# Performance work log

Measured on AMD Instinct MI355X. Metric: run time of the kernel, lower is better.

The kernel has to match this reference:

```python
import jax, jax.numpy as jnp
import numpy as np

R_MAX = 5.0
NUM_BESSEL = 8
P_CUT = 5.0
NUM_GRAPHS = 32
AVG_NEIGH = 16.0
N_NODES = 40000
N_EDGES = 640000
NUM_ELEM = 10
CHANNELS = 32
# map each of the 9 spherical-harmonic components (l=0..2) to its l index
L_OF_LM = jnp.array([0, 1, 1, 1, 2, 2, 2, 2, 2])


def _sph(u):
    # component-normalized real spherical harmonics up to l=2 on unit vectors
    x, y, z = u[:, 0], u[:, 1], u[:, 2]
    s3, s15, s5 = jnp.sqrt(3.0), jnp.sqrt(15.0), jnp.sqrt(5.0)
    return jnp.stack([
        jnp.ones_like(x),
        s3 * x, s3 * y, s3 * z,
        s15 * x * y, s15 * y * z,
        (s5 / 2.0) * (3.0 * z * z - 1.0),
        s15 * x * z, (s15 / 2.0) * (x * x - y * y),
    ], axis=-1)  # [E, 9]


def _radial(lengths):
    # Bessel radial basis with smooth polynomial cutoff (p = P_CUT)
    u = lengths / R_MAX
    n = jnp.arange(1, NUM_BESSEL + 1, dtype=lengths.dtype)
    bessel = jnp.sqrt(2.0 / R_MAX) * jnp.sin(n * jnp.pi * u[:, None]) / lengths[:, None]
    p = P_CUT
    fc = (1.0 - (p + 1.0) * (p + 2.0) / 2.0 * u ** p
          + p * (p + 2.0) * u ** (p + 1.0)
          - p * (p + 1.0) / 2.0 * u ** (p + 2.0))
    fc = jnp.where(u < 1.0, fc, 0.0)
    return bessel * fc[:, None]  # [E, NUM_BESSEL]


def _layer(h, sh, edge_feats, sender, receiver, W1, W2, n_nodes):
    # radial MLP -> per-(l, channel) tensor-product weights
    tp_w = jax.nn.silu(edge_feats @ W1) @ W2          # [E, 3*C]
    tp_w = tp_w.reshape(-1, 3, CHANNELS)[:, L_OF_LM]  # [E, 9, C]
    # equivariant message: sh outer sender scalar feats, radially weighted
    m = sh[:, :, None] * h[sender][:, None, :] * tp_w  # [E, 9, C]
    A = jax.ops.segment_sum(m, receiver, num_segments=n_nodes) / AVG_NEIGH
    return A.at[:, 0, :].add(h)  # residual on the scalar (l=0) part


def _energy(positions, node_attrs, shifts, atomic_energies, W_embed,
            W1a, W2a, Wr1, W1b, W2b, Wm1, Wm2, edge_index, batch):
    sender, receiver = edge_index[0], edge_index[1]
    vec = positions[receiver] - positions[sender] + shifts  # [E, 3]
    lengths = jnp.sqrt(jnp.maximum(jnp.sum(vec * vec, -1), 1e-12))
    sh = _sph(vec / lengths[:, None])
    ef = _radial(lengths)
    n_nodes = positions.shape[0]
    e0 = node_attrs @ atomic_energies       # per-atom reference energies
    h = node_attrs @ W_embed                # LinearNodeEmbeddingBlock
    A1 = _layer(h, sh, ef, sender, receiver, W1a, W2a, n_nodes)
    e1 = (A1[:, 0, :] @ Wr1)[:, 0]          # LinearReadoutBlock
    A2 = _layer(A1[:, 0, :], sh, ef, sender, receiver, W1b, W2b, n_nodes)
    e2 = (jax.nn.silu(A2[:, 0, :] @ Wm1) @ Wm2)[:, 0]  # NonLinearReadoutBlock
    node_energy = e0 + e1 + e2
    total = jax.ops.segment_sum(node_energy, batch, num_segments=NUM_GRAPHS)
    return total, node_energy


def setup_inputs() -> dict:
    key = jax.random.key(0)
    ks = jax.random.split(key, 16)
    node_z = jax.random.randint(ks[0], (N_NODES,), 0, NUM_ELEM)
    node_attrs = jax.nn.one_hot(node_z, NUM_ELEM, dtype=jnp.float32)
    return {
        "positions": jax.random.normal(ks[1], (N_NODES, 3), jnp.float32) * 2.0,
        "node_attrs": node_attrs,
        "shifts": jnp.zeros((N_EDGES, 3), jnp.float32),
        "atomic_energies": jax.random.normal(ks[2], (NUM_ELEM,), jnp.float32),
        "W_embed": jax.random.normal(ks[3], (NUM_ELEM, CHANNELS), jnp.float32) / np.sqrt(NUM_ELEM),
        "W1a": jax.random.normal(ks[4], (NUM_BESSEL, 64), jnp.float32) / np.sqrt(NUM_BESSEL),
        "W2a": jax.random.normal(ks[5], (64, 3 * CHANNELS), jnp.float32) / 8.0,
        "Wr1": jax.random.normal(ks[6], (CHANNELS, 1), jnp.float32) / np.sqrt(CHANNELS),
        "W1b": jax.random.normal(ks[7], (NUM_BESSEL, 64), jnp.float32) / np.sqrt(NUM_BESSEL),
        "W2b": jax.random.normal(ks[8], (64, 3 * CHANNELS), jnp.float32) / 8.0,
        "Wm1": jax.random.normal(ks[9], (CHANNELS, 16), jnp.float32) / np.sqrt(CHANNELS),
        "Wm2": jax.random.normal(ks[10], (16, 1), jnp.float32) / 4.0,
        "edge_index": jax.random.randint(ks[11], (2, N_EDGES), 0, N_NODES).astype(jnp.int32),
        "batch": jnp.sort(jax.random.randint(ks[12], (N_NODES,), 0, NUM_GRAPHS)).astype(jnp.int32),
    }


def reference(positions, node_attrs, shifts, atomic_energies, W_embed,
              W1a, W2a, Wr1, W1b, W2b, Wm1, Wm2, edge_index, batch):
    def esum(pos):
        total, node_e = _energy(pos, node_attrs, shifts, atomic_energies, W_embed,
                                W1a, W2a, Wr1, W1b, W2b, Wm1, Wm2, edge_index, batch)
        return jnp.sum(total), (total, node_e)

    (_, (total, node_e)), g = jax.value_and_grad(esum, has_aux=True)(positions)
    forces = -g  # forces = -dE/dpositions, as in get_outputs
    return total, node_e, forces
```

## Files before the change

kernel.cpp:

```cpp
#include <hip/hip_runtime.h>
#include <math.h>

constexpr float R_MAX   = 5.0f;
constexpr float INV_R   = 0.2f;
constexpr float PI_F    = 3.14159265358979323846f;
constexpr float C0      = 0.632455532033675866f;
constexpr float INV_AVG = 1.0f / 16.0f;
constexpr int   TBL     = 4096;
constexpr int   SCHUNK  = 512;

__device__ __forceinline__ float sigm(float x) { return 1.0f / (1.0f + __expf(-x)); }

__device__ __forceinline__ unsigned f2bf(float x) {
    unsigned u = __float_as_uint(x);
    u += 0x7fffu + ((u >> 16) & 1u);
    return u >> 16;
}
__device__ __forceinline__ void store_bf_row(unsigned short* dst, const float* v) {
    uint4* o = (uint4*)dst;
#pragma unroll
    for (int w = 0; w < 4; w++) {
        uint4 t;
        t.x = f2bf(v[8*w+0]) | (f2bf(v[8*w+1]) << 16);
        t.y = f2bf(v[8*w+2]) | (f2bf(v[8*w+3]) << 16);
        t.z = f2bf(v[8*w+4]) | (f2bf(v[8*w+5]) << 16);
        t.w = f2bf(v[8*w+6]) | (f2bf(v[8*w+7]) << 16);
        o[w] = t;
    }
}
__device__ __forceinline__ void load_bf_row(const unsigned short* src, float* v) {
    const uint4* p = (const uint4*)src;
#pragma unroll
    for (int w = 0; w < 4; w++) {
        uint4 t = p[w];
        v[8*w+0] = __uint_as_float(t.x << 16);
        v[8*w+1] = __uint_as_float(t.x & 0xffff0000u);
        v[8*w+2] = __uint_as_float(t.y << 16);
        v[8*w+3] = __uint_as_float(t.y & 0xffff0000u);
        v[8*w+4] = __uint_as_float(t.z << 16);
        v[8*w+5] = __uint_as_float(t.z & 0xffff0000u);
        v[8*w+6] = __uint_as_float(t.w << 16);
        v[8*w+7] = __uint_as_float(t.w & 0xffff0000u);
    }
}

__device__ __forceinline__ void radial_ef_d(float u, float invL, float* ef, float* dd) {
    float u2 = u * u, u4 = u2 * u2, u5 = u4 * u;
    float fc  = 1.f - 21.f * u5 + 35.f * u5 * u - 15.f * u5 * u2;
    float om  = 1.f - u;
    float fcp = -105.f * u4 * om * om;
    float sp, cp;
    sincosf(PI_F * u, &sp, &cp);
    float twoc = 2.f * cp;
    float a = C0 * invL;
    float s_nm1 = 0.f, s_n = sp, c_nm1 = 1.f, c_n = cp;
#pragma unroll
    for (int n = 1; n <= 8; n++) {
        ef[n - 1] = a * s_n * fc;
        dd[n - 1] = a * fc * ((float)n * PI_F * INV_R * c_n - s_n * invL)
                  + a * s_n * fcp * INV_R;
        if (n < 8) {
            float sn2 = twoc * s_n - s_nm1; s_nm1 = s_n; s_n = sn2;
            float cn2 = twoc * c_n - c_nm1; c_nm1 = c_n; c_n = cn2;
        }
    }
}

__global__ __launch_bounds__(256) void k_setup(
    const float* __restrict__ W1a, const float* __restrict__ W2a,
    const float* __restrict__ W1b, const float* __restrict__ W2b,
    float* __restrict__ twa, float* __restrict__ dta,
    float* __restrict__ twb, float* __restrict__ dtb,
    float* __restrict__ total,
    const float* __restrict__ attrs, const float* __restrict__ ae,
    const float* __restrict__ Wemb, float* __restrict__ h,
    unsigned short* __restrict__ hA1_bf, float* __restrict__ e0,
    float* __restrict__ A1, float* __restrict__ forces, int N,
    const float* __restrict__ pos, const float* __restrict__ shifts,
    const int* __restrict__ ei, int E,
    int* __restrict__ hist_r, int* __restrict__ hist_s,
    float4* __restrict__ urec,
    int nbt, int nbn)
{
    int b = blockIdx.x;
    if (b < nbt) {
        if (b == 0 && threadIdx.x < 32) total[threadIdx.x] = 0.f;
        int gid = b * 256 + threadIdx.x;
        if (gid >= (TBL + 1) * 16) return;
        int cg = gid & 7;
        int l  = (gid >> 3) & 1;
        int t  = gid >> 4;
        float u = fmaxf((float)t / (float)TBL, 1e-4f);
        float L = u * R_MAX;
        float invL = 1.f / L;
        float ef[8], dd[8], efu[8];
        radial_ef_d(u, invL, ef, dd);
#pragma unroll
        for (int k = 0; k < 8; k++) efu[k] = dd[k] * R_MAX;
        const float* W1 = l ? W1b : W1a;
        const float* W2 = l ? W2b : W2a;
        float*     tw_o = l ? twb : twa;
        float*     dt_o = l ? dtb : dta;
        float tw[4] = {0.f, 0.f, 0.f, 0.f};
        float dt[4] = {0.f, 0.f, 0.f, 0.f};
        for (int j = 0; j < 64; j++) {
            float s1 = 0.f, du = 0.f;
#pragma unroll
            for (int k = 0; k < 8; k++) {
                float w = W1[k * 64 + j];
                s1 += ef[k] * w; du += efu[k] * w;
            }
            float sg  = sigm(s1);
            float act = s1 * sg;
            float dj  = sg * (1.f + s1 * (1.f - sg)) * du;
            const float* w2 = W2 + j * 96 + cg * 4;
#pragma unroll
            for (int q = 0; q < 4; q++) {
                tw[q] += act * w2[q];
                dt[q] += dj * w2[q];
            }
        }
#pragma unroll
        for (int q = 0; q < 4; q++) {
            tw_o[(size_t)t * 32 + cg * 4 + q] = tw[q];
            dt_o[(size_t)t * 32 + cg * 4 + q] = dt[q];
        }
    } else if (b < nbt + nbn) {
        int i = (b - nbt) * 256 + threadIdx.x;
        if (i >= N) return;
        float a[10];
#pragma unroll
        for (int k = 0; k < 10; k++) a[k] = attrs[i * 10 + k];
        float e = 0.f;
#pragma unroll
        for (int k = 0; k < 10; k++) e += a[k] * ae[k];
        e0[i] = e;
        float v[32];
#pragma unroll
        for (int c = 0; c < 32; c++) {
            float t = 0.f;
#pragma unroll
            for (int k = 0; k < 10; k++) t += a[k] * Wemb[k * 32 + c];
            v[c] = t;
            h[i * 32 + c] = t;
            A1[i * 32 + c] = 0.f;
        }
        store_bf_row(hA1_bf + (size_t)i * 64, v);
        forces[3*i+0] = 0.f; forces[3*i+1] = 0.f; forces[3*i+2] = 0.f;
        hist_r[i] = 0; hist_s[i] = 0;
    } else {
        int e = (b - nbt - nbn) * 256 + threadIdx.x;
        if (e >= E) return;
        int s = ei[e], r = ei[E + e];
        float vx = pos[3*r+0] - pos[3*s+0] + shifts[3*e+0];
        float vy = pos[3*r+1] - pos[3*s+1] + shifts[3*e+1];
        float vz = pos[3*r+2] - pos[3*s+2] + shifts[3*e+2];
        float ss2 = vx*vx + vy*vy + vz*vz;
        float L = sqrtf(fmaxf(ss2, 1e-12f));
        if (L * INV_R < 1.f) {
            atomicAdd(&hist_r[r], 1);
            atomicAdd(&hist_s[s], 1);
            urec[e] = make_float4(vx, vy, vz,
                      __uint_as_float(((unsigned)s << 16) | (unsigned)r));
        } else {
            urec[e] = make_float4(0.f, 0.f, 0.f, __uint_as_float(0xFFFFFFFFu));
        }
    }
}

__global__ __launch_bounds__(256) void k_scan_a(
    const int* __restrict__ hist_r, const int* __restrict__ hist_s,
    int n, int nb, int* __restrict__ part)
{
    __shared__ int red[256];
    int b = blockIdx.x;
    const int* hist = (b < nb) ? hist_r : hist_s;
    int cb = (b < nb) ? b : b - nb;
    int base = cb * SCHUNK;
    int t = threadIdx.x;
    int i0 = base + 2 * t, i1 = i0 + 1;
    int sum = 0;
    if (i0 < n) sum += hist[i0];
    if (i1 < n) sum += hist[i1];
    red[t] = sum;
    __syncthreads();
    for (int off = 128; off > 0; off >>= 1) {
        if (t < off) red[t] += red[t + off];
        __syncthreads();
    }
    if (t == 0) part[b] = red[0];
}

__global__ __launch_bounds__(256) void k_scan_b(
    const int* __restrict__ part, int nb, int* __restrict__ bbase,
    int* __restrict__ cnt)
{
    __shared__ int buf[512];
    int t = threadIdx.x;
    for (int k = t; k < 2 * nb; k += 256) buf[k] = part[k];
    __syncthreads();
    if (t < 2) {
        int base = t * nb;
        int run = 0;
        for (int k = 0; k < nb; k++) {
            int v = buf[base + k];
            buf[base + k] = run;
            run += v;
        }
        if (t == 0) *cnt = run;
    }
    __syncthreads();
    for (int k = t; k < 2 * nb; k += 256) bbase[k] = buf[k];
}

__global__ __launch_bounds__(256) void k_scan_c(
    const int* __restrict__ hist_r, const int* __restrict__ hist_s,
    int n, int nb, const int* __restrict__ bbase,
    int* __restrict__ cur_r, int* __restrict__ cur_s)
{
    __shared__ int sc[256];
    int b = blockIdx.x;
    const int* hist = (b < nb) ? hist_r : hist_s;
    int*       cur  = (b < nb) ? cur_r : cur_s;
    int cb = (b < nb) ? b : b - nb;
    int base = cb * SCHUNK;
    int t = threadIdx.x;
    int i0 = base + 2 * t, i1 = i0 + 1;
    int e0 = (i0 < n) ? hist[i0] : 0;
    int e1 = (i1 < n) ? hist[i1] : 0;
    int ts = e0 + e1;
    sc[t] = ts;
    __syncthreads();
    for (int off = 1; off < 256; off <<= 1) {
        int v = (t >= off) ? sc[t - off] : 0;
        __syncthreads();
        sc[t] += v;
        __syncthreads();
    }
    int excl = sc[t] - ts + bbase[b];
    if (i0 < n) cur[i0] = excl;
    if (i1 < n) cur[i1] = excl + e0;
}

__global__ __launch_bounds__(256) void k_sort(
    const float4* __restrict__ urec, int E,
    int* __restrict__ cur_r, int* __restrict__ cur_s,
    float4* __restrict__ rrec, float4* __restrict__ srec,
    int* __restrict__ map_sr)
{
    int e = blockIdx.x * 256 + threadIdx.x;
    if (e >= E) return;
    float4 uv = urec[e];
    unsigned pk = __float_as_uint(uv.w);
    if (pk == 0xFFFFFFFFu) return;
    int r = (int)(pk & 0xffffu);
    int s = (int)(pk >> 16);
    int rp = atomicAdd(&cur_r[r], 1);
    int sp = atomicAdd(&cur_s[s], 1);
    rrec[rp] = uv;
    srec[sp] = make_float4(uv.x, uv.y, uv.z,
               __uint_as_float(((unsigned)r << 16) | (unsigned)s));
    map_sr[sp] = rp;
}

__global__ __launch_bounds__(256) void k_edge_mlp_t(
    const float4* __restrict__ rec, const int* __restrict__ cnt,
    const float* __restrict__ tw_tbl, const unsigned short* __restrict__ feat,
    int fstride, float* __restrict__ acc)
{
    __shared__ float m_lds[256][33];
    __shared__ int   dst_lds[256];

    int na = *cnt;
    int tid = threadIdx.x;
    int stride = gridDim.x * 256;

    for (int base = blockIdx.x * 256; base < na; base += stride) {
        int i = base + tid;
        int dst = -1;
        if (i < na) {
            float4 rv = rec[i];
            unsigned pk = __float_as_uint(rv.w);
            int gn = pk >> 16;
            dst = (int)(pk & 0xffffu);
            float ss2 = rv.x * rv.x + rv.y * rv.y + rv.z * rv.z;
            float L = sqrtf(fmaxf(ss2, 1e-12f));
            float x = fminf(L * (INV_R * (float)TBL), (float)TBL - 1e-3f);
            int   i0 = (int)x;
            float f  = x - (float)i0;

            float fbuf[32];
            load_bf_row(feat + (size_t)gn * fstride, fbuf);

            const float4* r0 = (const float4*)(tw_tbl + (size_t)i0 * 32);
            const float4* r1 = r0 + 8;
#pragma unroll
            for (int q = 0; q < 8; q++) {
                float4 a = r0[q], b = r1[q];
                m_lds[tid][4 * q + 0] = fbuf[4*q+0] * (a.x + f * (b.x - a.x));
                m_lds[tid][4 * q + 1] = fbuf[4*q+1] * (a.y + f * (b.y - a.y));
                m_lds[tid][4 * q + 2] = fbuf[4*q+2] * (a.z + f * (b.z - a.z));
                m_lds[tid][4 * q + 3] = fbuf[4*q+3] * (a.w + f * (b.w - a.w));
            }
        }
        dst_lds[tid] = dst;
        __syncthreads();

        int grp = tid >> 5;
        int c   = tid & 31;
        int b32 = grp * 32;
        int cur = -1; float run = 0.f;
        for (int k = 0; k < 32; k++) {
            int d = dst_lds[b32 + k];
            if (d != cur) {
                if (cur >= 0) unsafeAtomicAdd(&acc[(size_t)cur * 32 + c], run);
                cur = d;
                run = (d >= 0) ? m_lds[b32 + k][c] : 0.f;
            } else if (d >= 0) {
                run += m_lds[b32 + k][c];
            }
        }
        if (cur >= 0) unsafeAtomicAdd(&acc[(size_t)cur * 32 + c], run);
        __syncthreads();
    }
}

__global__ __launch_bounds__(256) void k_node1(
    const float* __restrict__ h, float* __restrict__ A1,
    unsigned short* __restrict__ hA1_bf,
    const float* __restrict__ Wr1, float* __restrict__ e1,
    float* __restrict__ A2g2, int N)
{
    int i = blockIdx.x * blockDim.x + threadIdx.x;
    if (i >= N) return;
    float dot = 0.f;
    float v[32];
#pragma unroll
    for (int c = 0; c < 32; c++) {
        float t = A1[i * 32 + c] * INV_AVG + h[i * 32 + c];
        v[c] = t;
        A1[i * 32 + c] = t;
        A2g2[i * 32 + c] = 0.f;
        dot += t * Wr1[c];
    }
    e1[i] = dot;
    store_bf_row(hA1_bf + (size_t)i * 64 + 32, v);
}

__global__ __launch_bounds__(256) void k_node2(
    float* __restrict__ A2g2, unsigned short* __restrict__ g2_bf,
    const float* __restrict__ A1,
    const float* __restrict__ Wm1, const float* __restrict__ Wm2,
    const float* __restrict__ e0, const float* __restrict__ e1,
    float* __restrict__ node_e, float* __restrict__ total,
    float* __restrict__ g1, const int* __restrict__ batch, int N)
{
    __shared__ float bins[32];
    if (threadIdx.x < 32) bins[threadIdx.x] = 0.f;
    __syncthreads();
    int i = blockIdx.x * blockDim.x + threadIdx.x;
    if (i < N) {
        float A2[32];
#pragma unroll
        for (int c = 0; c < 32; c++) {
            A2[c] = A2g2[i * 32 + c] * INV_AVG + A1[i * 32 + c];
            g1[i * 32 + c] = 0.f;
        }
        float z[16];
#pragma unroll
        for (int k = 0; k < 16; k++) {
            float v = 0.f;
#pragma unroll
            for (int c = 0; c < 32; c++) v += A2[c] * Wm1[c * 16 + k];
            z[k] = v;
        }
        float e2 = 0.f;
        float wk[16];
#pragma unroll
        for (int k = 0; k < 16; k++) {
            float sg = sigm(z[k]);
            float m2 = Wm2[k];
            e2 += z[k] * sg * m2;
            wk[k] = m2 * sg * (1.f + z[k] * (1.f - sg));
        }
        float g2v[32];
#pragma unroll
        for (int c = 0; c < 32; c++) {
            float v = 0.f;
#pragma unroll
            for (int k = 0; k < 16; k++) v += Wm1[c * 16 + k] * wk[k];
            g2v[c] = v;
            A2g2[i * 32 + c] = v;
        }
        store_bf_row(g2_bf + (size_t)i * 32, g2v);
        float ne = e0[i] + e1[i] + e2;
        node_e[i] = ne;
        atomicAdd(&bins[batch[i]], ne);
    }
    __syncthreads();
    if (threadIdx.x < 32) unsafeAtomicAdd(&total[threadIdx.x], bins[threadIdx.x]);
}

__global__ __launch_bounds__(256) void k_mlp3fb(
    const float4* __restrict__ rec, const int* __restrict__ cnt,
    const float* __restrict__ tw_tbl, const float* __restrict__ dt_tbl,
    const unsigned short* __restrict__ g2_bf,
    const unsigned short* __restrict__ hA1_bf,
    const int* __restrict__ map_sr,
    float* __restrict__ g1acc, float* __restrict__ dotb_buf)
{
    __shared__ float m_lds[256][33];
    __shared__ int   dst_lds[256];

    int na = *cnt;
    int tid = threadIdx.x;
    int stride = gridDim.x * 256;

    for (int base = blockIdx.x * 256; base < na; base += stride) {
        int i = base + tid;
        int dst = -1;
        if (i < na) {
            float4 rv = rec[i];
            unsigned pk = __float_as_uint(rv.w);
            int r = (int)(pk >> 16);
            dst = (int)(pk & 0xffffu);
            float ss2 = rv.x * rv.x + rv.y * rv.y + rv.z * rv.z;
            float L = sqrtf(fmaxf(ss2, 1e-12f));
            float x = fminf(L * (INV_R * (float)TBL), (float)TBL - 1e-3f);
            int   i0 = (int)x;
            float f  = x - (float)i0;

            float gb[32], ab[32];
            load_bf_row(g2_bf + (size_t)r * 32, gb);
            load_bf_row(hA1_bf + (size_t)dst * 64 + 32, ab);

            const float4* r0 = (const float4*)(tw_tbl + (size_t)i0 * 32);
            const float4* r1 = r0 + 8;
            const float4* d0 = (const float4*)(dt_tbl + (size_t)i0 * 32);
            const float4* d1 = d0 + 8;
            float dotb = 0.f;
#pragma unroll
            for (int q = 0; q < 8; q++) {
                float4 a = r0[q], b = r1[q], da = d0[q], db = d1[q];
                float t0 = a.x + f * (b.x - a.x);
                float t1 = a.y + f * (b.y - a.y);
                float t2 = a.z + f * (b.z - a.z);
                float t3 = a.w + f * (b.w - a.w);
                m_lds[tid][4*q+0] = gb[4*q+0] * t0;
                m_lds[tid][4*q+1] = gb[4*q+1] * t1;
                m_lds[tid][4*q+2] = gb[4*q+2] * t2;
                m_lds[tid][4*q+3] = gb[4*q+3] * t3;
                dotb += gb[4*q+0] * ab[4*q+0] * (da.x + f * (db.x - da.x))
                      + gb[4*q+1] * ab[4*q+1] * (da.y + f * (db.y - da.y))
                      + gb[4*q+2] * ab[4*q+2] * (da.z + f * (db.z - da.z))
                      + gb[4*q+3] * ab[4*q+3] * (da.w + f * (db.w - da.w));
            }
            dotb_buf[map_sr[i]] = dotb;
        }
        dst_lds[tid] = dst;
        __syncthreads();

        int grp = tid >> 5;
        int c   = tid & 31;
        int b32 = grp * 32;
        int cur = -1; float run = 0.f;
        for (int k = 0; k < 32; k++) {
            int d = dst_lds[b32 + k];
            if (d != cur) {
                if (cur >= 0) unsafeAtomicAdd(&g1acc[(size_t)cur * 32 + c], run);
                cur = d;
                run = (d >= 0) ? m_lds[b32 + k][c] : 0.f;
            } else if (d >= 0) {
                run += m_lds[b32 + k][c];
            }
        }
        if (cur >= 0) unsafeAtomicAdd(&g1acc[(size_t)cur * 32 + c], run);
        __syncthreads();
    }
}

__global__ __launch_bounds__(256) void k_force_ra(
    const float4* __restrict__ rec, const int* __restrict__ cnt,
    const float* __restrict__ dta,
    const unsigned short* __restrict__ hA1_bf,
    const float* __restrict__ g1acc, const float* __restrict__ g2,
    const float* __restrict__ Wr1, const float* __restrict__ dotb_buf,
    float* __restrict__ forces, float* __restrict__ sc_buf)
{
    __shared__ float f_lds[256][4];
    __shared__ int   dst_lds[256];

    int na = *cnt;
    int tid = threadIdx.x;
    int stride = gridDim.x * 256;
    const float4* w4 = (const float4*)Wr1;

    for (int base = blockIdx.x * 256; base < na; base += stride) {
        int i = base + tid;
        int dstf = -1;
        float fx = 0.f, fy = 0.f, fz = 0.f;

        if (i < na) {
            float4 rv = rec[i];
            unsigned pk = __float_as_uint(rv.w);
            int r = (int)(pk & 0xffffu);
            int s = (int)(pk >> 16);
            float vx = rv.x, vy = rv.y, vz = rv.z;
            float ss2 = vx * vx + vy * vy + vz * vz;
            float scv = 0.f;
            if (ss2 > 1e-12f) {
                float L = sqrtf(ss2);
                float invL = 1.f / L;
                float x = fminf(L * (INV_R * (float)TBL), (float)TBL - 1e-3f);
                int   i0 = (int)x;
                float f  = x - (float)i0;

                float hb[32];
                load_bf_row(hA1_bf + (size_t)s * 64, hb);

                const float4* a0 = (const float4*)(dta + (size_t)i0 * 32);
                const float4* a1 = a0 + 8;
                const float4* pa = (const float4*)(g1acc + (size_t)r * 32);
                const float4* pc = (const float4*)(g2 + (size_t)r * 32);

                float dot = dotb_buf[i];
#pragma unroll
                for (int q = 0; q < 8; q++) {
                    float4 ga = pa[q], gc = pc[q], wr = w4[q];
                    float4 t0 = a0[q], t1 = a1[q];
                    float g0 = ga.x * INV_AVG + gc.x + wr.x;
                    float g1v = ga.y * INV_AVG + gc.y + wr.y;
                    float g2v = ga.z * INV_AVG + gc.z + wr.z;
                    float g3 = ga.w * INV_AVG + gc.w + wr.w;
                    dot += g0 * hb[4*q+0] * (t0.x + f * (t1.x - t0.x))
                         + g1v * hb[4*q+1] * (t0.y + f * (t1.y - t0.y))
                         + g2v * hb[4*q+2] * (t0.z + f * (t1.z - t0.z))
                         + g3 * hb[4*q+3] * (t0.w + f * (t1.w - t0.w));
                }

                scv = INV_AVG * INV_R * dot * invL;
                fx = -scv * vx; fy = -scv * vy; fz = -scv * vz;
                dstf = r;
            }
            sc_buf[i] = scv;
        }
        f_lds[tid][0] = fx; f_lds[tid][1] = fy; f_lds[tid][2] = fz;
        dst_lds[tid] = dstf;
        __syncthreads();

        int grp = tid >> 5;
        int c   = tid & 31;
        if (c < 3) {
            int b32 = grp * 32;
            int cur = -1; float run = 0.f;
            for (int k = 0; k < 32; k++) {
                int d = dst_lds[b32 + k];
                if (d != cur) {
                    if (cur >= 0) unsafeAtomicAdd(&forces[3 * cur + c], run);
                    cur = d;
                    run = (d >= 0) ? f_lds[b32 + k][c] : 0.f;
                } else if (d >= 0) {
                    run += f_lds[b32 + k][c];
                }
            }
            if (cur >= 0) unsafeAtomicAdd(&forces[3 * cur + c], run);
        }
        __syncthreads();
    }
}

__global__ __launch_bounds__(256) void k_force_s2(
    const float4* __restrict__ rec, const int* __restrict__ cnt,
    const int* __restrict__ map_sr, const float* __restrict__ sc_buf,
    float* __restrict__ forces)
{
    __shared__ float f_lds[256][4];
    __shared__ int   dst_lds[256];

    int na = *cnt;
    int tid = threadIdx.x;
    int stride = gridDim.x * 256;

    for (int base = blockIdx.x * 256; base < na; base += stride) {
        int i = base + tid;
        int dstf = -1;
        float fx = 0.f, fy = 0.f, fz = 0.f;
        if (i < na) {
            float4 rv = rec[i];
            unsigned pk = __float_as_uint(rv.w);
            float scv = sc_buf[map_sr[i]];
            fx = scv * rv.x; fy = scv * rv.y; fz = scv * rv.z;
            dstf = (int)(pk & 0xffffu);
        }
        f_lds[tid][0] = fx; f_lds[tid][1] = fy; f_lds[tid][2] = fz;
        dst_lds[tid] = dstf;
        __syncthreads();

        int grp = tid >> 5;
        int c   = tid & 31;
        if (c < 3) {
            int b32 = grp * 32;
            int cur = -1; float run = 0.f;
            for (int k = 0; k < 32; k++) {
                int d = dst_lds[b32 + k];
                if (d != cur) {
                    if (cur >= 0) unsafeAtomicAdd(&forces[3 * cur + c], run);
                    cur = d;
                    run = (d >= 0) ? f_lds[b32 + k][c] : 0.f;
                } else if (d >= 0) {
                    run += f_lds[b32 + k][c];
                }
            }
            if (cur >= 0) unsafeAtomicAdd(&forces[3 * cur + c], run);
        }
        __syncthreads();
    }
}

extern "C" void kernel_launch(void* const* d_in, const int* in_sizes, int n_in,
                              void* d_out, int out_size, void* d_ws, size_t ws_size,
                              hipStream_t stream)
{
    const float* pos    = (const float*)d_in[0];
    const float* attrs  = (const float*)d_in[1];
    const float* shifts = (const float*)d_in[2];
    const float* ae     = (const float*)d_in[3];
    const float* Wemb   = (const float*)d_in[4];
    const float* W1a    = (const float*)d_in[5];
    const float* W2a    = (const float*)d_in[6];
    const float* Wr1    = (const float*)d_in[7];
    const float* W1b    = (const float*)d_in[8];
    const float* W2b    = (const float*)d_in[9];
    const float* Wm1    = (const float*)d_in[10];
    const float* Wm2    = (const float*)d_in[11];
    const int*   ei     = (const int*)d_in[12];
    const int*   batch  = (const int*)d_in[13];

    int N = in_sizes[13];
    int E = in_sizes[12] / 2;

    float* out    = (float*)d_out;
    float* total  = out;
    float* node_e = out + 32;
    float* forces = out + 32 + N;

    float* ws = (float*)d_ws;
    size_t NC = (size_t)N * 32;
    float* h    = ws;
    float* A1   = h  + NC;
    float* A2g2 = A1 + NC;
    float* g1   = A2g2 + NC;
    float* e0   = g1 + NC;
    float* e1   = e0 + N;
    int* hist_r = (int*)(e1 + N);
    int* hist_s = hist_r + N;
    int* cur_r  = hist_s + N;
    int* cur_s  = cur_r + N;
    int* cnt    = cur_s + N;
    size_t ioff = ((size_t)(cnt + 1 - (int*)ws) + 3) & ~(size_t)3;
    float4* rrec = (float4*)(ws + ioff);
    float4* srec = rrec + E;
    float* tbl  = (float*)(srec + E);
    size_t tstride = (size_t)(TBL + 1) * 32;
    float* twa = tbl;
    float* dta = twa + tstride;
    float* twb = dta + tstride;
    float* dtb = twb + tstride;
    int*   map_sr = (int*)(dtb + tstride);
    float* sc_buf = (float*)(map_sr + E);
    unsigned short* hA1_bf = (unsigned short*)(sc_buf + E);
    unsigned short* g2_bf  = hA1_bf + 2 * NC;
    int* part  = (int*)(g2_bf + NC);
    int* bbase = part + 1024;
    float* dotb_buf = (float*)(bbase + 1024);
    float4* urec = (float4*)A2g2;

    int nb_n = (N + 255) / 256;
    int nb_e = (E + 255) / 256;
    int nb_g = nb_e < 2048 ? nb_e : 2048;
    int nb_t = ((TBL + 1) * 16 + 255) / 256;
    int nbs  = (N + SCHUNK - 1) / SCHUNK;

    k_setup<<<nb_t + nb_n + nb_e, 256, 0, stream>>>(
        W1a, W2a, W1b, W2b, twa, dta, twb, dtb, total,
        attrs, ae, Wemb, h, hA1_bf, e0, A1, forces, N,
        pos, shifts, ei, E, hist_r, hist_s, urec, nb_t, nb_n);
    k_scan_a<<<2 * nbs, 256, 0, stream>>>(hist_r, hist_s, N, nbs, part);
    k_scan_b<<<1, 256, 0, stream>>>(part, nbs, bbase, cnt);
    k_scan_c<<<2 * nbs, 256, 0, stream>>>(hist_r, hist_s, N, nbs, bbase,
                                          cur_r, cur_s);
    k_sort<<<nb_e, 256, 0, stream>>>(urec, E, cur_r, cur_s, rrec, srec, map_sr);

    k_edge_mlp_t<<<nb_g, 256, 0, stream>>>(rrec, cnt, twa, hA1_bf, 64, A1);
    k_node1<<<nb_n, 256, 0, stream>>>(h, A1, hA1_bf, Wr1, e1, A2g2, N);
    k_edge_mlp_t<<<nb_g, 256, 0, stream>>>(rrec, cnt, twb, hA1_bf + 32, 64, A2g2);
    k_node2<<<nb_n, 256, 0, stream>>>(A2g2, g2_bf, A1, Wm1, Wm2, e0, e1,
                                      node_e, total, g1, batch, N);
    k_mlp3fb<<<nb_g, 256, 0, stream>>>(srec, cnt, twb, dtb, g2_bf, hA1_bf,
                                       map_sr, g1, dotb_buf);
    k_force_ra<<<nb_g, 256, 0, stream>>>(rrec, cnt, dta, hA1_bf,
                                         g1, A2g2, Wr1, dotb_buf,
                                         forces, sc_buf);
    k_force_s2<<<nb_g, 256, 0, stream>>>(srec, cnt, map_sr, sc_buf, forces);
}
```

Before: 271.0 us.

## Split edge sort and overlap sender-side sort with first edge MLP pass

The combined receiver/sender counting sort is split in two. Receiver placement now runs alone and records each edge's sorted position. Sender placement is done by extra blocks appended to the first edge-MLP kernel, so it runs alongside the first aggregation instead of before it. Each sort thread now handles two edges. This costs an extra per-edge index array plus a second read of the unsorted records, and the mixed grid may unbalance work across blocks.

```diff
diff --git a/kernel.cpp b/kernel.cpp
--- a/kernel.cpp
+++ b/kernel.cpp
@@ -242,25 +242,114 @@
     if (i1 < n) cur[i1] = excl + e0;
 }
 
-__global__ __launch_bounds__(256) void k_sort(
+__global__ __launch_bounds__(256) void k_sort_r(
     const float4* __restrict__ urec, int E,
-    int* __restrict__ cur_r, int* __restrict__ cur_s,
-    float4* __restrict__ rrec, float4* __restrict__ srec,
-    int* __restrict__ map_sr)
-{
-    int e = blockIdx.x * 256 + threadIdx.x;
-    if (e >= E) return;
-    float4 uv = urec[e];
-    unsigned pk = __float_as_uint(uv.w);
-    if (pk == 0xFFFFFFFFu) return;
-    int r = (int)(pk & 0xffffu);
-    int s = (int)(pk >> 16);
-    int rp = atomicAdd(&cur_r[r], 1);
-    int sp = atomicAdd(&cur_s[s], 1);
-    rrec[rp] = uv;
-    srec[sp] = make_float4(uv.x, uv.y, uv.z,
-               __uint_as_float(((unsigned)r << 16) | (unsigned)s));
-    map_sr[sp] = rp;
+    int* __restrict__ cur_r, float4* __restrict__ rrec,
+    int* __restrict__ rp_of_e)
+{
+    int base = blockIdx.x * 512;
+    int t = threadIdx.x;
+    int e0 = base + t, e1 = base + 256 + t;
+    float4 u0, u1;
+    unsigned p0 = 0xFFFFFFFFu, p1 = 0xFFFFFFFFu;
+    if (e0 < E) { u0 = urec[e0]; p0 = __float_as_uint(u0.w); }
+    if (e1 < E) { u1 = urec[e1]; p1 = __float_as_uint(u1.w); }
+    int rp0 = -1, rp1 = -1;
+    if (p0 != 0xFFFFFFFFu) rp0 = atomicAdd(&cur_r[p0 & 0xffffu], 1);
+    if (p1 != 0xFFFFFFFFu) rp1 = atomicAdd(&cur_r[p1 & 0xffffu], 1);
+    if (rp0 >= 0) { rrec[rp0] = u0; rp_of_e[e0] = rp0; }
+    if (rp1 >= 0) { rrec[rp1] = u1; rp_of_e[e1] = rp1; }
+}
+
+__global__ __launch_bounds__(256) void k_mlp1_sorts(
+    const float4* __restrict__ rec, const int* __restrict__ cnt,
+    const float* __restrict__ tw_tbl, const unsigned short* __restrict__ feat,
+    float* __restrict__ acc,
+    const float4* __restrict__ urec, int E, int* __restrict__ cur_s,
+    float4* __restrict__ srec, int* __restrict__ map_sr,
+    const int* __restrict__ rp_of_e, int nb_g)
+{
+    __shared__ float m_lds[256][33];
+    __shared__ int   dst_lds[256];
+
+    int b = blockIdx.x;
+    int tid = threadIdx.x;
+
+    if (b >= nb_g) {
+        int base = (b - nb_g) * 512;
+        int e0 = base + tid, e1 = base + 256 + tid;
+        float4 u0, u1;
+        unsigned p0 = 0xFFFFFFFFu, p1 = 0xFFFFFFFFu;
+        if (e0 < E) { u0 = urec[e0]; p0 = __float_as_uint(u0.w); }
+        if (e1 < E) { u1 = urec[e1]; p1 = __float_as_uint(u1.w); }
+        int sp0 = -1, sp1 = -1;
+        if (p0 != 0xFFFFFFFFu) sp0 = atomicAdd(&cur_s[p0 >> 16], 1);
+        if (p1 != 0xFFFFFFFFu) sp1 = atomicAdd(&cur_s[p1 >> 16], 1);
+        if (sp0 >= 0) {
+            unsigned r = p0 & 0xffffu, s = p0 >> 16;
+            srec[sp0] = make_float4(u0.x, u0.y, u0.z,
+                        __uint_as_float((r << 16) | s));
+            map_sr[sp0] = rp_of_e[e0];
+        }
+        if (sp1 >= 0) {
+            unsigned r = p1 & 0xffffu, s = p1 >> 16;
+            srec[sp1] = make_float4(u1.x, u1.y, u1.z,
+                        __uint_as_float((r << 16) | s));
+            map_sr[sp1] = rp_of_e[e1];
+        }
+        return;
+    }
+
+    int na = *cnt;
+    int stride = nb_g * 256;
+    for (int base = b * 256; base < na; base += stride) {
+        int i = base + tid;
+        int dst = -1;
+        if (i < na) {
+            float4 rv = rec[i];
+            unsigned pk = __float_as_uint(rv.w);
+            int gn = pk >> 16;
+            dst = (int)(pk & 0xffffu);
+            float ss2 = rv.x * rv.x + rv.y * rv.y + rv.z * rv.z;
+            float L = sqrtf(fmaxf(ss2, 1e-12f));
+            float x = fminf(L * (INV_R * (float)TBL), (float)TBL - 1e-3f);
+            int   i0 = (int)x;
+            float f  = x - (float)i0;
+
+            float fbuf[32];
+            load_bf_row(feat + (size_t)gn * 64, fbuf);
+
+            const float4* r0 = (const float4*)(tw_tbl + (size_t)i0 * 32);
+            const float4* r1 = r0 + 8;
+#pragma unroll
+            for (int q = 0; q < 8; q++) {
+                float4 a = r0[q], bb = r1[q];
+                m_lds[tid][4 * q + 0] = fbuf[4*q+0] * (a.x + f * (bb.x - a.x));
+                m_lds[tid][4 * q + 1] = fbuf[4*q+1] * (a.y + f * (bb.y - a.y));
+                m_lds[tid][4 * q + 2] = fbuf[4*q+2] * (a.z + f * (bb.z - a.z));
+                m_lds[tid][4 * q + 3] = fbuf[4*q+3] * (a.w + f * (bb.w - a.w));
+            }
+        }
+        dst_lds[tid] = dst;
+        __syncthreads();
+
+        int grp = tid >> 5;
+        int c   = tid & 31;
+        int b32 = grp * 32;
+        int cur = -1; float run = 0.f;
+        for (int k = 0; k < 32; k++) {
+            int d = dst_lds[b32 + k];
+            if (d != cur) {
+                if (cur >= 0) unsafeAtomicAdd(&acc[(size_t)cur * 32 + c], run);
+                cur = d;
+                run = (d >= 0) ? m_lds[b32 + k][c] : 0.f;
+            } else if (d >= 0) {
+                run += m_lds[b32 + k][c];
+            }
+        }
+        if (cur >= 0) unsafeAtomicAdd(&acc[(size_t)cur * 32 + c], run);
+        __syncthreads();
+    }
 }
 
 __global__ __launch_bounds__(256) void k_edge_mlp_t(
@@ -673,13 +762,15 @@
     int* part  = (int*)(g2_bf + NC);
     int* bbase = part + 1024;
     float* dotb_buf = (float*)(bbase + 1024);
+    int*   rp_of_e  = (int*)(dotb_buf + E);
     float4* urec = (float4*)A2g2;
 
-    int nb_n = (N + 255) / 256;
-    int nb_e = (E + 255) / 256;
-    int nb_g = nb_e < 2048 ? nb_e : 2048;
-    int nb_t = ((TBL + 1) * 16 + 255) / 256;
-    int nbs  = (N + SCHUNK - 1) / SCHUNK;
+    int nb_n  = (N + 255) / 256;
+    int nb_e  = (E + 255) / 256;
+    int nb_e2 = (E + 511) / 512;
+    int nb_g  = nb_e < 2048 ? nb_e : 2048;
+    int nb_t  = ((TBL + 1) * 16 + 255) / 256;
+    int nbs   = (N + SCHUNK - 1) / SCHUNK;
 
     k_setup<<<nb_t + nb_n + nb_e, 256, 0, stream>>>(
         W1a, W2a, W1b, W2b, twa, dta, twb, dtb, total,
@@ -689,9 +780,11 @@
     k_scan_b<<<1, 256, 0, stream>>>(part, nbs, bbase, cnt);
     k_scan_c<<<2 * nbs, 256, 0, stream>>>(hist_r, hist_s, N, nbs, bbase,
                                           cur_r, cur_s);
-    k_sort<<<nb_e, 256, 0, stream>>>(urec, E, cur_r, cur_s, rrec, srec, map_sr);
-
-    k_edge_mlp_t<<<nb_g, 256, 0, stream>>>(rrec, cnt, twa, hA1_bf, 64, A1);
+    k_sort_r<<<nb_e2, 256, 0, stream>>>(urec, E, cur_r, rrec, rp_of_e);
+
+    k_mlp1_sorts<<<nb_g + nb_e2, 256, 0, stream>>>(
+        rrec, cnt, twa, hA1_bf, A1,
+        urec, E, cur_s, srec, map_sr, rp_of_e, nb_g);
     k_node1<<<nb_n, 256, 0, stream>>>(h, A1, hA1_bf, Wr1, e1, A2g2, N);
     k_edge_mlp_t<<<nb_g, 256, 0, stream>>>(rrec, cnt, twb, hA1_bf + 32, 64, A2g2);
     k_node2<<<nb_n, 256, 0, stream>>>(A2g2, g2_bf, A1, Wm1, Wm2, e0, e1,
```

New measurement: 268.6 us. Within noise of the previous version (-0.9%).
